# Kernel tuning notes

Hardware: AMD Instinct MI355X
Metric: run time of the kernel (lower is better)

The kernel has to match this reference:

```python
import jax, jax.numpy as jnp
import numpy as np

N_QUBITS = 6
N_LAYERS = 2
FEATURE_DIMS = [768, 512, 1024]
BATCH = 16384
PI = np.float32(np.pi)
C64 = jnp.complex64


def _ry(t):
    c = jnp.cos(t / 2).astype(C64)
    s = jnp.sin(t / 2).astype(C64)
    return jnp.stack([jnp.stack([c, -s], -1), jnp.stack([s, c], -1)], -2)


def _rx(t):
    c = jnp.cos(t / 2).astype(C64)
    s = (-1j * jnp.sin(t / 2).astype(C64))
    return jnp.stack([jnp.stack([c, s], -1), jnp.stack([s, c], -1)], -2)


def _rz(t):
    e = jnp.exp(-0.5j * t.astype(C64))
    z = jnp.zeros_like(e)
    return jnp.stack([jnp.stack([e, z], -1), jnp.stack([z, jnp.conj(e)], -1)], -2)


def _apply_1q(state, gate, wire):
    # state: [B, 2,...,2]; gate: [2,2] (shared) or [B,2,2] (per-sample)
    s = jnp.moveaxis(state, wire + 1, -1)
    shp = s.shape
    s = s.reshape(shp[0], -1, 2)
    if gate.ndim == 2:
        s = jnp.einsum('ij,bkj->bki', gate, s)
    else:
        s = jnp.einsum('bij,bkj->bki', gate, s)
    return jnp.moveaxis(s.reshape(shp), -1, wire + 1)


def _apply_cnot(state, control, target):
    s = jnp.moveaxis(state, (control + 1, target + 1), (1, 2))
    s = jnp.stack([s[:, 0], s[:, 1, ::-1]], axis=1)
    return jnp.moveaxis(s, (1, 2), (control + 1, target + 1))


def _apply_cry(state, theta, control, target):
    s = jnp.moveaxis(state, (control + 1, target + 1), (1, 2))
    g = _ry(theta)  # [2,2]
    c1 = jnp.einsum('ij,bj...->bi...', g, s[:, 1])
    s = jnp.stack([s[:, 0], c1], axis=1)
    return jnp.moveaxis(s, (1, 2), (control + 1, target + 1))


def run_circuit(angles, qw):
    # angles: [B, n_qubits] encoding RY angles; qw: [n_layers, n_qubits, 3]
    B = angles.shape[0]
    n = N_QUBITS
    state = jnp.zeros((B,) + (2,) * n, C64).at[(slice(None),) + (0,) * n].set(1.0)
    # encoding: sequential RYs on a wire compose to RY(sum of angles); RY(0) is identity
    for i in range(n):
        state = _apply_1q(state, _ry(angles[:, i]), i)
    for l in range(N_LAYERS):
        for i in range(n):
            state = _apply_1q(state, _rx(qw[l, i, 0]), i)
            state = _apply_1q(state, _ry(qw[l, i, 1]), i)
            state = _apply_1q(state, _rz(qw[l, i, 2]), i)
        for i in range(n - 1):
            state = _apply_cnot(state, i, i + 1)
        if n > 2:
            state = _apply_cnot(state, 0, n - 1)
        for i in range(0, n - 1, 2):
            state = _apply_cry(state, qw[l, i, 1], i, i + 1)
    probs = state.real ** 2 + state.imag ** 2  # [B, 2,...,2]
    z = [(jnp.take(probs, 0, axis=i + 1) - jnp.take(probs, 1, axis=i + 1)).reshape(B, -1).sum(-1)
         for i in range(n)]
    return jnp.stack(z, axis=-1)  # [B, n_qubits]


def setup_inputs() -> dict:
    key = jax.random.key(0)
    ks = jax.random.split(key, 10)
    inp = {}
    for m, d in enumerate(FEATURE_DIMS):
        inp[f'feat{m}'] = jax.random.normal(ks[m], (BATCH, d), jnp.float32)
        inp[f'W{m}'] = jax.random.normal(ks[3 + m], (d, N_QUBITS), jnp.float32) / np.sqrt(d)
        inp[f'b{m}'] = jnp.zeros((N_QUBITS,), jnp.float32)
    inp['qw'] = 0.1 * jax.random.normal(ks[6], (N_LAYERS, N_QUBITS, 3), jnp.float32)
    inp['fusion_logits'] = jnp.ones((len(FEATURE_DIMS),), jnp.float32) / len(FEATURE_DIMS)
    return inp


def reference(feat0, feat1, feat2, W0, b0, W1, b1, W2, b2, qw, fusion_logits):
    fw = jax.nn.softmax(fusion_logits)
    q0 = jnp.tanh(feat0 @ W0 + b0)  # [B, n_qubits]
    q1 = jnp.tanh(feat1 @ W1 + b1)
    q2 = jnp.tanh(feat2 @ W2 + b2)
    angles = PI * (fw[0] * q0 + fw[1] * q1 + fw[2] * q2)
    return run_circuit(angles, qw)
```

## Files before the change

### kernel.cpp

```cpp
#include <hip/hip_runtime.h>

#define PI_F 3.14159265358979323846f

#define D0 768
#define D1 512
#define D2 1024
#define WT_FLOATS 13824
#define U_OFF   WT_FLOATS
#define CRY_OFF (WT_FLOATS + 48)


__global__ void prep_kernel(const float* __restrict__ W0, const float* __restrict__ W1,
                            const float* __restrict__ W2, const float* __restrict__ qw,
                            float* __restrict__ ws) {
    int t = blockIdx.x * 256 + threadIdx.x;
    if (t < 4608) {
        int j = t / 768, k = t - j * 768;
        ws[t] = W0[k * 6 + j];
    } else if (t < 7680) {
        int u = t - 4608, j = u / 512, k = u - j * 512;
        ws[t] = W1[k * 6 + j];
    } else if (t < WT_FLOATS) {
        int u = t - 7680, j = u / 1024, k = u - j * 1024;
        ws[t] = W2[k * 6 + j];
    } else if (t < WT_FLOATS + 12) {
        int g = t - WT_FLOATS;
        float ca, sa, cb, sb, cc, sc;
        sincosf(0.5f * qw[g * 3 + 0], &sa, &ca);
        sincosf(0.5f * qw[g * 3 + 1], &sb, &cb);
        sincosf(0.5f * qw[g * 3 + 2], &sc, &cc);
        float m00r = cb * ca, m00i = sb * sa;
        float m01r = -sb * ca, m01i = -cb * sa;
        float* u4 = ws + U_OFF + g * 4;
        u4[0] = m00r * cc + m00i * sc;
        u4[1] = m00i * cc - m00r * sc;
        u4[2] = m01r * cc + m01i * sc;
        u4[3] = m01i * cc - m01r * sc;
    } else if (t < WT_FLOATS + 18) {
        int k = t - WT_FLOATS - 12;
        int l = k / 3, i = (k - l * 3) * 2;
        float c, s;
        sincosf(0.5f * qw[(l * 6 + i) * 3 + 1], &s, &c);
        ws[CRY_OFF + k * 2 + 0] = c;
        ws[CRY_OFF + k * 2 + 1] = s;
    }
}


template<int CTRL>
__device__ __forceinline__ float dppmov(float v) {
    return __int_as_float(__builtin_amdgcn_update_dpp(0, __float_as_int(v), CTRL, 0xF, 0xF, true));
}
template<int PAT>
__device__ __forceinline__ float swzf(float v) {
    return __int_as_float(__builtin_amdgcn_ds_swizzle(__float_as_int(v), PAT));
}

template<int M>
__device__ __forceinline__ float xsh(float v) {
    if constexpr (M == 1)       return dppmov<0xB1>(v);
    else if constexpr (M == 2)  return dppmov<0x4E>(v);
    else if constexpr (M == 4)  return swzf<0x101F>(v);
    else if constexpr (M == 8)  return dppmov<0x128>(v);
    else if constexpr (M == 16) return swzf<0x401F>(v);
    else                        return __shfl_xor(v, 32, 64);
}

__device__ __forceinline__ float pl16_sum(float v) {
#if __has_builtin(__builtin_amdgcn_permlane16_swap)
    auto r = __builtin_amdgcn_permlane16_swap(__float_as_uint(v), __float_as_uint(v), false, false);
    return __uint_as_float(r[0]) + __uint_as_float(r[1]);
#else
    return v + swzf<0x401F>(v);
#endif
}
__device__ __forceinline__ float pl32_sum(float v) {
#if __has_builtin(__builtin_amdgcn_permlane32_swap)
    auto r = __builtin_amdgcn_permlane32_swap(__float_as_uint(v), __float_as_uint(v), false, false);
    return __uint_as_float(r[0]) + __uint_as_float(r[1]);
#else
    return v + __shfl_xor(v, 32, 64);
#endif
}

__device__ __forceinline__ float bfly_sum(float v) {
    v += dppmov<0xB1>(v);
    v += dppmov<0x4E>(v);
    v += swzf<0x101F>(v);
    v += dppmov<0x128>(v);
    v = pl16_sum(v);
    v = pl32_sum(v);
    return v;
}

__device__ __forceinline__ float fast_tanh(float x) {
    float e = __expf(2.0f * x);
    return 1.0f - 2.0f / (e + 1.0f);
}

__device__ __forceinline__ float dot4(float4 a, float4 w, float acc) {
    return fmaf(a.x, w.x, fmaf(a.y, w.y, fmaf(a.z, w.z, fmaf(a.w, w.w, acc))));
}


template<int M>
__device__ __forceinline__ void gateU(float (&re)[2], float (&im)[2], int lane,
                                      float ar, float ai, float br, float bi) {
    const bool hi = (lane & M) != 0;
    const float Ai = hi ? -ai : ai;
    const float Br = hi ? -br : br;
#pragma unroll
    for (int s = 0; s < 2; ++s) {
        float pre = xsh<M>(re[s]);
        float pim = xsh<M>(im[s]);
        float nr = ar * re[s] - Ai * im[s] + Br * pre - bi * pim;
        float ni = ar * im[s] + Ai * re[s] + Br * pim + bi * pre;
        re[s] = nr; im[s] = ni;
    }
}

template<int MC, int MT>
__device__ __forceinline__ void gateCRY(float (&re)[2], float (&im)[2], int lane, float c, float sn) {
    const bool c1 = (lane & MC) != 0;
    const float sg = (lane & MT) ? sn : -sn;
#pragma unroll
    for (int s = 0; s < 2; ++s) {
        float pre = xsh<MT>(re[s]);
        float pim = xsh<MT>(im[s]);
        float nr = fmaf(c, re[s], sg * pre);
        float ni = fmaf(c, im[s], sg * pim);
        re[s] = c1 ? nr : re[s];
        im[s] = c1 ? ni : im[s];
    }
}

template<int I>
__device__ __forceinline__ void l1gate(float (&re)[2], float (&im)[2], int lane,
                                       const float* __restrict__ ws) {
    constexpr int M = 32 >> I;
    const float ar = ws[U_OFF + (6 + I) * 4 + 0];
    const float ai = ws[U_OFF + (6 + I) * 4 + 1];
    const float br = ws[U_OFF + (6 + I) * 4 + 2];
    const float bi = ws[U_OFF + (6 + I) * 4 + 3];
    gateU<M>(re, im, lane, ar, ai, br, bi);
}

template<int L, int P>
__device__ __forceinline__ void cryGate(float (&re)[2], float (&im)[2], int lane,
                                        const float* __restrict__ ws) {
    constexpr int MC = 32 >> (2 * P);
    constexpr int MT = 16 >> (2 * P);
    const float c = ws[CRY_OFF + (L * 3 + P) * 2 + 0];
    const float s = ws[CRY_OFF + (L * 3 + P) * 2 + 1];
    gateCRY<MC, MT>(re, im, lane, c, s);
}

__device__ __forceinline__ void buildState(const float (&ang)[6], int lane,
                                           const float* __restrict__ ws,
                                           float& reO, float& imO) {
    float pr, pi;
#pragma unroll
    for (int i = 0; i < 6; ++i) {
        float cq, sq;
        __sincosf(0.5f * ang[i], &sq, &cq);
        const float ar = ws[U_OFF + i * 4 + 0];
        const float ai = ws[U_OFF + i * 4 + 1];
        const float br = ws[U_OFF + i * 4 + 2];
        const float bi = ws[U_OFF + i * 4 + 3];
        float vloR = ar * cq + br * sq;
        float vloI = ai * cq + bi * sq;
        float vhiR = ar * sq - br * cq;
        float vhiI = bi * cq - ai * sq;
        bool hi = (lane & (32 >> i)) != 0;
        float vr = hi ? vhiR : vloR;
        float vi = hi ? vhiI : vloI;
        if (i == 0) { pr = vr; pi = vi; }
        else { float t = pr * vr - pi * vi; pi = pr * vi + pi * vr; pr = t; }
    }
    reO = pr; imO = pi;
}


__global__ __launch_bounds__(256, 3) void qf_main(
    const float* __restrict__ f0, const float* __restrict__ b0,
    const float* __restrict__ f1, const float* __restrict__ b1,
    const float* __restrict__ f2, const float* __restrict__ b2,
    const float* __restrict__ fl, const float* __restrict__ ws,
    float* __restrict__ out)
{
    const int lane = threadIdx.x & 63;
    const int wave = blockIdx.x * 4 + (threadIdx.x >> 6);
    const int s0 = wave * 2;

    const float4* __restrict__ xA0 = (const float4*)(f0 + (size_t)s0 * D0);
    const float4* __restrict__ xB0 = (const float4*)(f0 + (size_t)(s0 + 1) * D0);
    const float4* __restrict__ xA1 = (const float4*)(f1 + (size_t)s0 * D1);
    const float4* __restrict__ xB1 = (const float4*)(f1 + (size_t)(s0 + 1) * D1);
    const float4* __restrict__ xA2 = (const float4*)(f2 + (size_t)s0 * D2);
    const float4* __restrict__ xB2 = (const float4*)(f2 + (size_t)(s0 + 1) * D2);

    float4 xa0 = xA0[lane], xa1 = xA0[64 + lane], xa2 = xA0[128 + lane];
    float4 xb0 = xB0[lane], xb1 = xB0[64 + lane], xb2 = xB0[128 + lane];
    float4 xa3 = xA1[lane], xa4 = xA1[64 + lane];
    float4 xb3 = xB1[lane], xb4 = xB1[64 + lane];
    float4 xa5 = xA2[lane], xa6 = xA2[64 + lane], xa7 = xA2[128 + lane], xa8 = xA2[192 + lane];
    float4 xb5 = xB2[lane], xb6 = xB2[64 + lane], xb7 = xB2[128 + lane], xb8 = xB2[192 + lane];

    float l0 = fl[0], l1 = fl[1], l2 = fl[2];
    float mx = fmaxf(l0, fmaxf(l1, l2));
    float e0 = __expf(l0 - mx), e1 = __expf(l1 - mx), e2 = __expf(l2 - mx);
    float inv = 1.0f / (e0 + e1 + e2);
    float fw0 = e0 * inv, fw1 = e1 * inv, fw2 = e2 * inv;

    const float4* __restrict__ w4 = (const float4*)ws;
    float accA[6], accB[6];
    float angA[6], angB[6];

#pragma unroll
    for (int j = 0; j < 6; ++j) {
        float4 w0 = w4[j * 192 + lane];
        float4 w1 = w4[j * 192 + 64 + lane];
        float4 w2 = w4[j * 192 + 128 + lane];
        float a = 0.f, b = 0.f;
        a = dot4(xa0, w0, a); a = dot4(xa1, w1, a); a = dot4(xa2, w2, a);
        b = dot4(xb0, w0, b); b = dot4(xb1, w1, b); b = dot4(xb2, w2, b);
        accA[j] = a; accB[j] = b;
    }
#pragma unroll
    for (int j = 0; j < 6; ++j) {
        angA[j] = fw0 * fast_tanh(bfly_sum(accA[j]) + b0[j]);
        angB[j] = fw0 * fast_tanh(bfly_sum(accB[j]) + b0[j]);
    }

#pragma unroll
    for (int j = 0; j < 6; ++j) {
        float4 w0 = w4[1152 + j * 128 + lane];
        float4 w1 = w4[1152 + j * 128 + 64 + lane];
        float a = 0.f, b = 0.f;
        a = dot4(xa3, w0, a); a = dot4(xa4, w1, a);
        b = dot4(xb3, w0, b); b = dot4(xb4, w1, b);
        accA[j] = a; accB[j] = b;
    }
#pragma unroll
    for (int j = 0; j < 6; ++j) {
        angA[j] += fw1 * fast_tanh(bfly_sum(accA[j]) + b1[j]);
        angB[j] += fw1 * fast_tanh(bfly_sum(accB[j]) + b1[j]);
    }

#pragma unroll
    for (int j = 0; j < 6; ++j) {
        float4 w0 = w4[1920 + j * 256 + lane];
        float4 w1 = w4[1920 + j * 256 + 64 + lane];
        float4 w2 = w4[1920 + j * 256 + 128 + lane];
        float4 w3 = w4[1920 + j * 256 + 192 + lane];
        float a = 0.f, b = 0.f;
        a = dot4(xa5, w0, a); a = dot4(xa6, w1, a); a = dot4(xa7, w2, a); a = dot4(xa8, w3, a);
        b = dot4(xb5, w0, b); b = dot4(xb6, w1, b); b = dot4(xb7, w2, b); b = dot4(xb8, w3, b);
        accA[j] = a; accB[j] = b;
    }
#pragma unroll
    for (int j = 0; j < 6; ++j) {
        angA[j] = PI_F * (angA[j] + fw2 * fast_tanh(bfly_sum(accA[j]) + b2[j]));
        angB[j] = PI_F * (angB[j] + fw2 * fast_tanh(bfly_sum(accB[j]) + b2[j]));
    }

    const int sigma = lane ^ ((lane >> 1) & 0x1F) ^ ((lane >> 5) & 1);

    float re[2], im[2];
    buildState(angA, lane, ws, re[0], im[0]);
    buildState(angB, lane, ws, re[1], im[1]);

    re[0] = __shfl(re[0], sigma, 64); im[0] = __shfl(im[0], sigma, 64);
    re[1] = __shfl(re[1], sigma, 64); im[1] = __shfl(im[1], sigma, 64);
    cryGate<0,0>(re, im, lane, ws); cryGate<0,1>(re, im, lane, ws); cryGate<0,2>(re, im, lane, ws);

    l1gate<0>(re, im, lane, ws); l1gate<1>(re, im, lane, ws); l1gate<2>(re, im, lane, ws);
    l1gate<3>(re, im, lane, ws); l1gate<4>(re, im, lane, ws); l1gate<5>(re, im, lane, ws);
    re[0] = __shfl(re[0], sigma, 64); im[0] = __shfl(im[0], sigma, 64);
    re[1] = __shfl(re[1], sigma, 64); im[1] = __shfl(im[1], sigma, 64);
    cryGate<1,0>(re, im, lane, ws); cryGate<1,1>(re, im, lane, ws); cryGate<1,2>(re, im, lane, ws);

#pragma unroll
    for (int s = 0; s < 2; ++s) {
        float p = fmaf(re[s], re[s], im[s] * im[s]);
        float q;
        q = xsh<1>(p);  p = (lane & 1)  ? (q - p) : (p + q);
        q = xsh<2>(p);  p = (lane & 2)  ? (q - p) : (p + q);
        q = xsh<4>(p);  p = (lane & 4)  ? (q - p) : (p + q);
        q = xsh<8>(p);  p = (lane & 8)  ? (q - p) : (p + q);
        q = xsh<16>(p); p = (lane & 16) ? (q - p) : (p + q);
        q = xsh<32>(p); p = (lane & 32) ? (q - p) : (p + q);
        if (__popc(lane) == 1)
            out[(size_t)(s0 + s) * 6 + (6 - __ffs(lane))] = p;
    }
}

extern "C" void kernel_launch(void* const* d_in, const int* in_sizes, int n_in,
                              void* d_out, int out_size, void* d_ws, size_t ws_size,
                              hipStream_t stream) {
    const float* f0 = (const float*)d_in[0];
    const float* W0 = (const float*)d_in[1];
    const float* b0 = (const float*)d_in[2];
    const float* f1 = (const float*)d_in[3];
    const float* W1 = (const float*)d_in[4];
    const float* b1 = (const float*)d_in[5];
    const float* f2 = (const float*)d_in[6];
    const float* W2 = (const float*)d_in[7];
    const float* b2 = (const float*)d_in[8];
    const float* qw = (const float*)d_in[9];
    const float* fl = (const float*)d_in[10];
    float* out = (float*)d_out;
    float* ws = (float*)d_ws;

    prep_kernel<<<55, 256, 0, stream>>>(W0, W1, W2, qw, ws);
    qf_main<<<2048, 256, 0, stream>>>(f0, b0, f1, b1, f2, b2, fl, ws, out);
}
```

Before: 48.37 us.

## Defer feat2 loads, batch all wave reductions, raise occupancy target to 4

Loads of the third feature block now happen only after the first projection finishes, with sched_barriers fencing them so fewer float4 registers are live at once. All 36 partial dot products are kept and reduced together, one butterfly stage at a time, which lets the DPP and permlane steps interleave instead of running as dependent chains. The launch bound moves from 3 to 4 waves per SIMD to raise occupancy. The risk is register spilling from the 36-element array under the tighter register budget, and less overlap because the feat2 loads start later.

```diff
diff --git a/kernel.cpp b/kernel.cpp
--- a/kernel.cpp
+++ b/kernel.cpp
@@ -83,16 +83,6 @@
 #endif
 }
 
-__device__ __forceinline__ float bfly_sum(float v) {
-    v += dppmov<0xB1>(v);
-    v += dppmov<0x4E>(v);
-    v += swzf<0x101F>(v);
-    v += dppmov<0x128>(v);
-    v = pl16_sum(v);
-    v = pl32_sum(v);
-    return v;
-}
-
 __device__ __forceinline__ float fast_tanh(float x) {
     float e = __expf(2.0f * x);
     return 1.0f - 2.0f / (e + 1.0f);
@@ -181,7 +171,7 @@
 }
 
 
-__global__ __launch_bounds__(256, 3) void qf_main(
+__global__ __launch_bounds__(256, 4) void qf_main(
     const float* __restrict__ f0, const float* __restrict__ b0,
     const float* __restrict__ f1, const float* __restrict__ b1,
     const float* __restrict__ f2, const float* __restrict__ b2,
@@ -203,8 +193,7 @@
     float4 xb0 = xB0[lane], xb1 = xB0[64 + lane], xb2 = xB0[128 + lane];
     float4 xa3 = xA1[lane], xa4 = xA1[64 + lane];
     float4 xb3 = xB1[lane], xb4 = xB1[64 + lane];
-    float4 xa5 = xA2[lane], xa6 = xA2[64 + lane], xa7 = xA2[128 + lane], xa8 = xA2[192 + lane];
-    float4 xb5 = xB2[lane], xb6 = xB2[64 + lane], xb7 = xB2[128 + lane], xb8 = xB2[192 + lane];
+    __builtin_amdgcn_sched_barrier(0);
 
     float l0 = fl[0], l1 = fl[1], l2 = fl[2];
     float mx = fmaxf(l0, fmaxf(l1, l2));
@@ -213,8 +202,7 @@
     float fw0 = e0 * inv, fw1 = e1 * inv, fw2 = e2 * inv;
 
     const float4* __restrict__ w4 = (const float4*)ws;
-    float accA[6], accB[6];
-    float angA[6], angB[6];
+    float r[36];
 
 #pragma unroll
     for (int j = 0; j < 6; ++j) {
@@ -224,13 +212,12 @@
         float a = 0.f, b = 0.f;
         a = dot4(xa0, w0, a); a = dot4(xa1, w1, a); a = dot4(xa2, w2, a);
         b = dot4(xb0, w0, b); b = dot4(xb1, w1, b); b = dot4(xb2, w2, b);
-        accA[j] = a; accB[j] = b;
-    }
-#pragma unroll
-    for (int j = 0; j < 6; ++j) {
-        angA[j] = fw0 * fast_tanh(bfly_sum(accA[j]) + b0[j]);
-        angB[j] = fw0 * fast_tanh(bfly_sum(accB[j]) + b0[j]);
-    }
+        r[j] = a; r[6 + j] = b;
+    }
+
+    float4 xa5 = xA2[lane], xa6 = xA2[64 + lane], xa7 = xA2[128 + lane], xa8 = xA2[192 + lane];
+    float4 xb5 = xB2[lane], xb6 = xB2[64 + lane], xb7 = xB2[128 + lane], xb8 = xB2[192 + lane];
+    __builtin_amdgcn_sched_barrier(0);
 
 #pragma unroll
     for (int j = 0; j < 6; ++j) {
@@ -239,12 +226,7 @@
         float a = 0.f, b = 0.f;
         a = dot4(xa3, w0, a); a = dot4(xa4, w1, a);
         b = dot4(xb3, w0, b); b = dot4(xb4, w1, b);
-        accA[j] = a; accB[j] = b;
-    }
-#pragma unroll
-    for (int j = 0; j < 6; ++j) {
-        angA[j] += fw1 * fast_tanh(bfly_sum(accA[j]) + b1[j]);
-        angB[j] += fw1 * fast_tanh(bfly_sum(accB[j]) + b1[j]);
+        r[12 + j] = a; r[18 + j] = b;
     }
 
 #pragma unroll
@@ -256,12 +238,33 @@
         float a = 0.f, b = 0.f;
         a = dot4(xa5, w0, a); a = dot4(xa6, w1, a); a = dot4(xa7, w2, a); a = dot4(xa8, w3, a);
         b = dot4(xb5, w0, b); b = dot4(xb6, w1, b); b = dot4(xb7, w2, b); b = dot4(xb8, w3, b);
-        accA[j] = a; accB[j] = b;
-    }
+        r[24 + j] = a; r[30 + j] = b;
+    }
+
+#pragma unroll
+    for (int k = 0; k < 36; ++k) r[k] += dppmov<0xB1>(r[k]);
+#pragma unroll
+    for (int k = 0; k < 36; ++k) r[k] += dppmov<0x4E>(r[k]);
+#pragma unroll
+    for (int k = 0; k < 36; ++k) r[k] += swzf<0x101F>(r[k]);
+#pragma unroll
+    for (int k = 0; k < 36; ++k) r[k] += dppmov<0x128>(r[k]);
+#pragma unroll
+    for (int k = 0; k < 36; ++k) r[k] = pl16_sum(r[k]);
+#pragma unroll
+    for (int k = 0; k < 36; ++k) r[k] = pl32_sum(r[k]);
+
+    float angA[6], angB[6];
 #pragma unroll
     for (int j = 0; j < 6; ++j) {
-        angA[j] = PI_F * (angA[j] + fw2 * fast_tanh(bfly_sum(accA[j]) + b2[j]));
-        angB[j] = PI_F * (angB[j] + fw2 * fast_tanh(bfly_sum(accB[j]) + b2[j]));
+        float tA0 = fast_tanh(r[j]      + b0[j]);
+        float tB0 = fast_tanh(r[6 + j]  + b0[j]);
+        float tA1 = fast_tanh(r[12 + j] + b1[j]);
+        float tB1 = fast_tanh(r[18 + j] + b1[j]);
+        float tA2 = fast_tanh(r[24 + j] + b2[j]);
+        float tB2 = fast_tanh(r[30 + j] + b2[j]);
+        angA[j] = PI_F * (fw0 * tA0 + fw1 * tA1 + fw2 * tA2);
+        angB[j] = PI_F * (fw0 * tB0 + fw1 * tB1 + fw2 * tB2);
     }
 
     const int sigma = lane ^ ((lane >> 1) & 0x1F) ^ ((lane >> 5) & 1);
```

Result: faster. 46.39 us (-4.1%).

## Split projection into bf16x3 MFMA GEMM kernel and separate circuit kernel

Applied to the files above, without the earlier changes.

Moves the feature projection from per-wave FP32 dot products with butterfly reductions onto MFMA 16x16x32 bf16 instructions. It keeps near-FP32 accuracy by splitting inputs and weights into hi/lo bf16 parts and issuing three MFMAs per step. The tanh and softmax fusion is done in the GEMM epilogue, which writes angles to a workspace buffer. A second kernel then runs the quantum circuit from those angles. This adds an extra launch and a global round trip for the angles. The GEMM also uses only 256 blocks, which may limit how much memory bandwidth it can draw on, since the workload is bound by reading the features.

```diff
diff --git a/kernel.cpp b/kernel.cpp
--- a/kernel.cpp
+++ b/kernel.cpp
@@ -5,44 +5,171 @@
 #define D0 768
 #define D1 512
 #define D2 1024
-#define WT_FLOATS 13824
-#define U_OFF   WT_FLOATS
-#define CRY_OFF (WT_FLOATS + 48)
-
-
-__global__ void prep_kernel(const float* __restrict__ W0, const float* __restrict__ W1,
-                            const float* __restrict__ W2, const float* __restrict__ qw,
-                            float* __restrict__ ws) {
-    int t = blockIdx.x * 256 + threadIdx.x;
-    if (t < 4608) {
-        int j = t / 768, k = t - j * 768;
-        ws[t] = W0[k * 6 + j];
-    } else if (t < 7680) {
-        int u = t - 4608, j = u / 512, k = u - j * 512;
-        ws[t] = W1[k * 6 + j];
-    } else if (t < WT_FLOATS) {
-        int u = t - 7680, j = u / 1024, k = u - j * 1024;
-        ws[t] = W2[k * 6 + j];
-    } else if (t < WT_FLOATS + 12) {
-        int g = t - WT_FLOATS;
+#define KTOT 2304
+
+#define U_OFF   73728
+#define CRY_OFF 73776
+#define ANG_OFF 73792
+
+typedef short short8 __attribute__((ext_vector_type(8)));
+typedef float f32x4 __attribute__((ext_vector_type(4)));
+typedef unsigned int uint4v __attribute__((ext_vector_type(4)));
+
+
+__global__ void prep_bt(const float* __restrict__ W0, const float* __restrict__ W1,
+                        const float* __restrict__ W2, unsigned short* __restrict__ bt_hi,
+                        unsigned short* __restrict__ bt_lo) {
+    int k = blockIdx.x * 256 + threadIdx.x;
+    int c = blockIdx.y;
+    float v = 0.0f;
+    if (c < 6)       { if (k < 768)              v = W0[k * 6 + c]; }
+    else if (c < 12) { if (k >= 768 && k < 1280) v = W1[(k - 768) * 6 + (c - 6)]; }
+    else if (c < 18) { if (k >= 1280)            v = W2[(k - 1280) * 6 + (c - 12)]; }
+    unsigned int u = __float_as_uint(v);
+    float hif = __uint_as_float(u & 0xFFFF0000u);
+    float lo = v - hif;
+    bt_hi[c * KTOT + k] = (unsigned short)(u >> 16);
+    bt_lo[c * KTOT + k] = (unsigned short)(__float_as_uint(lo) >> 16);
+}
+
+__global__ void prep_consts(const float* __restrict__ qw, float* __restrict__ wsf) {
+    int t = threadIdx.x;
+    if (t < 12) {
+        int g = t;
         float ca, sa, cb, sb, cc, sc;
         sincosf(0.5f * qw[g * 3 + 0], &sa, &ca);
         sincosf(0.5f * qw[g * 3 + 1], &sb, &cb);
         sincosf(0.5f * qw[g * 3 + 2], &sc, &cc);
         float m00r = cb * ca, m00i = sb * sa;
         float m01r = -sb * ca, m01i = -cb * sa;
-        float* u4 = ws + U_OFF + g * 4;
+        float* u4 = wsf + U_OFF + g * 4;
         u4[0] = m00r * cc + m00i * sc;
         u4[1] = m00i * cc - m00r * sc;
         u4[2] = m01r * cc + m01i * sc;
         u4[3] = m01i * cc - m01r * sc;
-    } else if (t < WT_FLOATS + 18) {
-        int k = t - WT_FLOATS - 12;
+    } else if (t < 18) {
+        int k = t - 12;
         int l = k / 3, i = (k - l * 3) * 2;
         float c, s;
         sincosf(0.5f * qw[(l * 6 + i) * 3 + 1], &s, &c);
-        ws[CRY_OFF + k * 2 + 0] = c;
-        ws[CRY_OFF + k * 2 + 1] = s;
+        wsf[CRY_OFF + k * 2 + 0] = c;
+        wsf[CRY_OFF + k * 2 + 1] = s;
+    }
+}
+
+
+__device__ __forceinline__ unsigned int pkhi(float x, float y) {
+    return (__float_as_uint(x) >> 16) | (__float_as_uint(y) & 0xFFFF0000u);
+}
+__device__ __forceinline__ float truncbf(float x) {
+    return __uint_as_float(__float_as_uint(x) & 0xFFFF0000u);
+}
+__device__ __forceinline__ void split8(float4 x0, float4 x1, short8& hi, short8& lo) {
+    uint4v h, l;
+    h[0] = pkhi(x0.x, x0.y); h[1] = pkhi(x0.z, x0.w);
+    h[2] = pkhi(x1.x, x1.y); h[3] = pkhi(x1.z, x1.w);
+    l[0] = pkhi(x0.x - truncbf(x0.x), x0.y - truncbf(x0.y));
+    l[1] = pkhi(x0.z - truncbf(x0.z), x0.w - truncbf(x0.w));
+    l[2] = pkhi(x1.x - truncbf(x1.x), x1.y - truncbf(x1.y));
+    l[3] = pkhi(x1.z - truncbf(x1.z), x1.w - truncbf(x1.w));
+    hi = __builtin_bit_cast(short8, h);
+    lo = __builtin_bit_cast(short8, l);
+}
+__device__ __forceinline__ f32x4 mfma16(short8 a, short8 b, f32x4 c) {
+    return __builtin_amdgcn_mfma_f32_16x16x32_bf16(a, b, c, 0, 0, 0);
+}
+
+__device__ __forceinline__ float fast_tanh(float x) {
+    float e = __expf(2.0f * x);
+    return 1.0f - 2.0f / (e + 1.0f);
+}
+
+__global__ __launch_bounds__(256) void gemm_kernel(
+    const float* __restrict__ f0, const float* __restrict__ f1, const float* __restrict__ f2,
+    const float* __restrict__ b0, const float* __restrict__ b1, const float* __restrict__ b2,
+    const float* __restrict__ fl, const unsigned short* __restrict__ bt_hi,
+    const unsigned short* __restrict__ bt_lo, float* __restrict__ ang_out)
+{
+    const int lane = threadIdx.x & 63;
+    const int wave = blockIdx.x * 4 + (threadIdx.x >> 6);
+    const int row_base = wave * 16;
+    const int c = lane & 15;
+    const int kh = lane >> 4;
+
+    f32x4 acc0 = {0.f, 0.f, 0.f, 0.f};
+    f32x4 acc1 = {0.f, 0.f, 0.f, 0.f};
+
+    const float* a0 = f0 + (size_t)(row_base + c) * D0 + kh * 8;
+    const float* a1 = f1 + (size_t)(row_base + c) * D1 + kh * 8;
+    const float* a2 = f2 + (size_t)(row_base + c) * D2 + kh * 8;
+    const unsigned short* bh = bt_hi + c * KTOT + kh * 8;
+    const unsigned short* bl = bt_lo + c * KTOT + kh * 8;
+
+#pragma unroll 4
+    for (int t = 0; t < 24; ++t) {
+        float4 x0 = *(const float4*)(a0 + t * 32);
+        float4 x1 = *(const float4*)(a0 + t * 32 + 4);
+        short8 ahi, alo; split8(x0, x1, ahi, alo);
+        short8 bh0 = *(const short8*)(bh + t * 32);
+        short8 bl0 = *(const short8*)(bl + t * 32);
+        acc0 = mfma16(ahi, bh0, acc0);
+        acc0 = mfma16(alo, bh0, acc0);
+        acc0 = mfma16(ahi, bl0, acc0);
+    }
+#pragma unroll 4
+    for (int t = 0; t < 16; ++t) {
+        float4 x0 = *(const float4*)(a1 + t * 32);
+        float4 x1 = *(const float4*)(a1 + t * 32 + 4);
+        short8 ahi, alo; split8(x0, x1, ahi, alo);
+        short8 bh0 = *(const short8*)(bh + 768 + t * 32);
+        short8 bl0 = *(const short8*)(bl + 768 + t * 32);
+        acc0 = mfma16(ahi, bh0, acc0);
+        acc0 = mfma16(alo, bh0, acc0);
+        acc0 = mfma16(ahi, bl0, acc0);
+    }
+#pragma unroll 4
+    for (int t = 0; t < 32; ++t) {
+        float4 x0 = *(const float4*)(a2 + t * 32);
+        float4 x1 = *(const float4*)(a2 + t * 32 + 4);
+        short8 ahi, alo; split8(x0, x1, ahi, alo);
+        short8 bh0 = *(const short8*)(bh + 1280 + t * 32);
+        short8 bl0 = *(const short8*)(bl + 1280 + t * 32);
+        short8 bh1 = *(const short8*)(bh + 16 * KTOT + 1280 + t * 32);
+        short8 bl1 = *(const short8*)(bl + 16 * KTOT + 1280 + t * 32);
+        acc0 = mfma16(ahi, bh0, acc0);
+        acc0 = mfma16(alo, bh0, acc0);
+        acc0 = mfma16(ahi, bl0, acc0);
+        acc1 = mfma16(ahi, bh1, acc1);
+        acc1 = mfma16(alo, bh1, acc1);
+        acc1 = mfma16(ahi, bl1, acc1);
+    }
+
+    float l0 = fl[0], l1 = fl[1], l2 = fl[2];
+    float mx = fmaxf(l0, fmaxf(l1, l2));
+    float e0 = __expf(l0 - mx), e1 = __expf(l1 - mx), e2 = __expf(l2 - mx);
+    float inv = 1.0f / (e0 + e1 + e2);
+    float fw0 = e0 * inv, fw1 = e1 * inv, fw2 = e2 * inv;
+
+    float bia, fwm;
+    if (c < 6)       { bia = b0[c];      fwm = fw0; }
+    else if (c < 12) { bia = b1[c - 6];  fwm = fw1; }
+    else             { bia = b2[c - 12]; fwm = fw2; }
+    float bia1 = (c < 2) ? b2[4 + c] : 0.f;
+
+    float ang4[4];
+#pragma unroll
+    for (int r = 0; r < 4; ++r) {
+        float vj = fwm * fast_tanh(acc0[r] + bia);
+        float v1 = (c < 2) ? fw2 * fast_tanh(acc1[r] + bia1) : 0.f;
+        float m2v = (c >= 12) ? vj : v1;
+        float sh6  = __shfl(vj,  (lane & 48) | ((c + 6) & 15), 64);
+        float shm2 = __shfl(m2v, (lane & 48) | ((c < 4 ? c + 12 : c - 4) & 15), 64);
+        ang4[r] = PI_F * (vj + sh6 + shm2);
+    }
+    if (c < 6) {
+#pragma unroll
+        for (int r = 0; r < 4; ++r)
+            ang_out[(size_t)(row_base + kh * 4 + r) * 6 + c] = ang4[r];
     }
 }
 
@@ -55,7 +182,6 @@
 __device__ __forceinline__ float swzf(float v) {
     return __int_as_float(__builtin_amdgcn_ds_swizzle(__float_as_int(v), PAT));
 }
-
 template<int M>
 __device__ __forceinline__ float xsh(float v) {
     if constexpr (M == 1)       return dppmov<0xB1>(v);
@@ -66,43 +192,6 @@
     else                        return __shfl_xor(v, 32, 64);
 }
 
-__device__ __forceinline__ float pl16_sum(float v) {
-#if __has_builtin(__builtin_amdgcn_permlane16_swap)
-    auto r = __builtin_amdgcn_permlane16_swap(__float_as_uint(v), __float_as_uint(v), false, false);
-    return __uint_as_float(r[0]) + __uint_as_float(r[1]);
-#else
-    return v + swzf<0x401F>(v);
-#endif
-}
-__device__ __forceinline__ float pl32_sum(float v) {
-#if __has_builtin(__builtin_amdgcn_permlane32_swap)
-    auto r = __builtin_amdgcn_permlane32_swap(__float_as_uint(v), __float_as_uint(v), false, false);
-    return __uint_as_float(r[0]) + __uint_as_float(r[1]);
-#else
-    return v + __shfl_xor(v, 32, 64);
-#endif
-}
-
-__device__ __forceinline__ float bfly_sum(float v) {
-    v += dppmov<0xB1>(v);
-    v += dppmov<0x4E>(v);
-    v += swzf<0x101F>(v);
-    v += dppmov<0x128>(v);
-    v = pl16_sum(v);
-    v = pl32_sum(v);
-    return v;
-}
-
-__device__ __forceinline__ float fast_tanh(float x) {
-    float e = __expf(2.0f * x);
-    return 1.0f - 2.0f / (e + 1.0f);
-}
-
-__device__ __forceinline__ float dot4(float4 a, float4 w, float acc) {
-    return fmaf(a.x, w.x, fmaf(a.y, w.y, fmaf(a.z, w.z, fmaf(a.w, w.w, acc))));
-}
-
-
 template<int M>
 __device__ __forceinline__ void gateU(float (&re)[2], float (&im)[2], int lane,
                                       float ar, float ai, float br, float bi) {
@@ -138,21 +227,16 @@
 __device__ __forceinline__ void l1gate(float (&re)[2], float (&im)[2], int lane,
                                        const float* __restrict__ ws) {
     constexpr int M = 32 >> I;
-    const float ar = ws[U_OFF + (6 + I) * 4 + 0];
-    const float ai = ws[U_OFF + (6 + I) * 4 + 1];
-    const float br = ws[U_OFF + (6 + I) * 4 + 2];
-    const float bi = ws[U_OFF + (6 + I) * 4 + 3];
-    gateU<M>(re, im, lane, ar, ai, br, bi);
-}
-
+    gateU<M>(re, im, lane, ws[U_OFF + (6 + I) * 4 + 0], ws[U_OFF + (6 + I) * 4 + 1],
+             ws[U_OFF + (6 + I) * 4 + 2], ws[U_OFF + (6 + I) * 4 + 3]);
+}
 template<int L, int P>
 __device__ __forceinline__ void cryGate(float (&re)[2], float (&im)[2], int lane,
                                         const float* __restrict__ ws) {
     constexpr int MC = 32 >> (2 * P);
     constexpr int MT = 16 >> (2 * P);
-    const float c = ws[CRY_OFF + (L * 3 + P) * 2 + 0];
-    const float s = ws[CRY_OFF + (L * 3 + P) * 2 + 1];
-    gateCRY<MC, MT>(re, im, lane, c, s);
+    gateCRY<MC, MT>(re, im, lane, ws[CRY_OFF + (L * 3 + P) * 2 + 0],
+                    ws[CRY_OFF + (L * 3 + P) * 2 + 1]);
 }
 
 __device__ __forceinline__ void buildState(const float (&ang)[6], int lane,
@@ -180,89 +264,17 @@
     reO = pr; imO = pi;
 }
 
-
-__global__ __launch_bounds__(256, 3) void qf_main(
-    const float* __restrict__ f0, const float* __restrict__ b0,
-    const float* __restrict__ f1, const float* __restrict__ b1,
-    const float* __restrict__ f2, const float* __restrict__ b2,
-    const float* __restrict__ fl, const float* __restrict__ ws,
-    float* __restrict__ out)
+__global__ __launch_bounds__(256, 8) void circuit_kernel(
+    const float* __restrict__ ws, const float* __restrict__ ang_buf, float* __restrict__ out)
 {
     const int lane = threadIdx.x & 63;
     const int wave = blockIdx.x * 4 + (threadIdx.x >> 6);
     const int s0 = wave * 2;
 
-    const float4* __restrict__ xA0 = (const float4*)(f0 + (size_t)s0 * D0);
-    const float4* __restrict__ xB0 = (const float4*)(f0 + (size_t)(s0 + 1) * D0);
-    const float4* __restrict__ xA1 = (const float4*)(f1 + (size_t)s0 * D1);
-    const float4* __restrict__ xB1 = (const float4*)(f1 + (size_t)(s0 + 1) * D1);
-    const float4* __restrict__ xA2 = (const float4*)(f2 + (size_t)s0 * D2);
-    const float4* __restrict__ xB2 = (const float4*)(f2 + (size_t)(s0 + 1) * D2);
-
-    float4 xa0 = xA0[lane], xa1 = xA0[64 + lane], xa2 = xA0[128 + lane];
-    float4 xb0 = xB0[lane], xb1 = xB0[64 + lane], xb2 = xB0[128 + lane];
-    float4 xa3 = xA1[lane], xa4 = xA1[64 + lane];
-    float4 xb3 = xB1[lane], xb4 = xB1[64 + lane];
-    float4 xa5 = xA2[lane], xa6 = xA2[64 + lane], xa7 = xA2[128 + lane], xa8 = xA2[192 + lane];
-    float4 xb5 = xB2[lane], xb6 = xB2[64 + lane], xb7 = xB2[128 + lane], xb8 = xB2[192 + lane];
-
-    float l0 = fl[0], l1 = fl[1], l2 = fl[2];
-    float mx = fmaxf(l0, fmaxf(l1, l2));
-    float e0 = __expf(l0 - mx), e1 = __expf(l1 - mx), e2 = __expf(l2 - mx);
-    float inv = 1.0f / (e0 + e1 + e2);
-    float fw0 = e0 * inv, fw1 = e1 * inv, fw2 = e2 * inv;
-
-    const float4* __restrict__ w4 = (const float4*)ws;
-    float accA[6], accB[6];
+    const float* aA = ang_buf + (size_t)s0 * 6;
     float angA[6], angB[6];
-
-#pragma unroll
-    for (int j = 0; j < 6; ++j) {
-        float4 w0 = w4[j * 192 + lane];
-        float4 w1 = w4[j * 192 + 64 + lane];
-        float4 w2 = w4[j * 192 + 128 + lane];
-        float a = 0.f, b = 0.f;
-        a = dot4(xa0, w0, a); a = dot4(xa1, w1, a); a = dot4(xa2, w2, a);
-        b = dot4(xb0, w0, b); b = dot4(xb1, w1, b); b = dot4(xb2, w2, b);
-        accA[j] = a; accB[j] = b;
-    }
-#pragma unroll
-    for (int j = 0; j < 6; ++j) {
-        angA[j] = fw0 * fast_tanh(bfly_sum(accA[j]) + b0[j]);
-        angB[j] = fw0 * fast_tanh(bfly_sum(accB[j]) + b0[j]);
-    }
-
-#pragma unroll
-    for (int j = 0; j < 6; ++j) {
-        float4 w0 = w4[1152 + j * 128 + lane];
-        float4 w1 = w4[1152 + j * 128 + 64 + lane];
-        float a = 0.f, b = 0.f;
-        a = dot4(xa3, w0, a); a = dot4(xa4, w1, a);
-        b = dot4(xb3, w0, b); b = dot4(xb4, w1, b);
-        accA[j] = a; accB[j] = b;
-    }
-#pragma unroll
-    for (int j = 0; j < 6; ++j) {
-        angA[j] += fw1 * fast_tanh(bfly_sum(accA[j]) + b1[j]);
-        angB[j] += fw1 * fast_tanh(bfly_sum(accB[j]) + b1[j]);
-    }
-
-#pragma unroll
-    for (int j = 0; j < 6; ++j) {
-        float4 w0 = w4[1920 + j * 256 + lane];
-        float4 w1 = w4[1920 + j * 256 + 64 + lane];
-        float4 w2 = w4[1920 + j * 256 + 128 + lane];
-        float4 w3 = w4[1920 + j * 256 + 192 + lane];
-        float a = 0.f, b = 0.f;
-        a = dot4(xa5, w0, a); a = dot4(xa6, w1, a); a = dot4(xa7, w2, a); a = dot4(xa8, w3, a);
-        b = dot4(xb5, w0, b); b = dot4(xb6, w1, b); b = dot4(xb7, w2, b); b = dot4(xb8, w3, b);
-        accA[j] = a; accB[j] = b;
-    }
-#pragma unroll
-    for (int j = 0; j < 6; ++j) {
-        angA[j] = PI_F * (angA[j] + fw2 * fast_tanh(bfly_sum(accA[j]) + b2[j]));
-        angB[j] = PI_F * (angB[j] + fw2 * fast_tanh(bfly_sum(accB[j]) + b2[j]));
-    }
+#pragma unroll
+    for (int j = 0; j < 6; ++j) { angA[j] = aA[j]; angB[j] = aA[6 + j]; }
 
     const int sigma = lane ^ ((lane >> 1) & 0x1F) ^ ((lane >> 5) & 1);
 
@@ -310,8 +322,14 @@
     const float* qw = (const float*)d_in[9];
     const float* fl = (const float*)d_in[10];
     float* out = (float*)d_out;
-    float* ws = (float*)d_ws;
-
-    prep_kernel<<<55, 256, 0, stream>>>(W0, W1, W2, qw, ws);
-    qf_main<<<2048, 256, 0, stream>>>(f0, b0, f1, b1, f2, b2, fl, ws, out);
-}
+
+    unsigned short* bt_hi = (unsigned short*)d_ws;
+    unsigned short* bt_lo = bt_hi + 73728;
+    float* wsf = (float*)d_ws;
+    float* ang = wsf + ANG_OFF;
+
+    prep_bt<<<dim3(9, 32), 256, 0, stream>>>(W0, W1, W2, bt_hi, bt_lo);
+    prep_consts<<<1, 64, 0, stream>>>(qw, wsf);
+    gemm_kernel<<<256, 256, 0, stream>>>(f0, f1, f2, b0, b1, b2, fl, bt_hi, bt_lo, ang);
+    circuit_kernel<<<2048, 256, 0, stream>>>(wsf, ang, out);
+}
```

New measurement: 78.61 us. 1.63x slower.
